# Kernel tuning notes

Measured on AMD Instinct MI355X. Metric: run time of the kernel, lower is better.

The kernel has to match this reference:

```python
import jax, jax.numpy as jnp
import numpy as np

B, N, D, H = 2, 2048, 256, 4
DH = D // H  # 64
ALPHA_DIV = 0.01
LN_EPS = 1e-5


def _split_heads(t):
    # [B, N, D] -> [B, H, N, DH]
    b, n, _ = t.shape
    return t.reshape(b, n, H, DH).transpose(0, 2, 1, 3)


def _merge_heads(t):
    # [B, H, N, DH] -> [B, N, D]
    b, h, n, d = t.shape
    return t.transpose(0, 2, 1, 3).reshape(b, n, h * d)


def setup_inputs() -> dict:
    key = jax.random.key(0)
    ks = jax.random.split(key, 20)
    p = lambda k, shape: (jax.random.normal(k, shape, dtype=jnp.float32) * 0.02)
    return {
        "x0": jax.random.normal(ks[0], (B, N, D), dtype=jnp.float32),
        "x1": jax.random.normal(ks[1], (B, N, D), dtype=jnp.float32),
        "cross_mask0": jax.random.uniform(ks[2], (B, 1, N), dtype=jnp.float32),
        "cross_mask1": jax.random.uniform(ks[3], (B, 1, N), dtype=jnp.float32),
        # weights stored as [in, out]
        "Wqk": p(ks[4], (D, D)), "bqk": jnp.zeros((D,), jnp.float32),
        "Wv": p(ks[5], (D, D)), "bv": jnp.zeros((D,), jnp.float32),
        "Wo": p(ks[6], (D, D)), "bo": jnp.zeros((D,), jnp.float32),
        "W1": p(ks[7], (2 * D, 2 * D)), "b1": jnp.zeros((2 * D,), jnp.float32),
        "ln_g": jnp.ones((2 * D,), jnp.float32), "ln_b": jnp.zeros((2 * D,), jnp.float32),
        "W2": p(ks[8], (2 * D, D)), "b2": jnp.zeros((D,), jnp.float32),
    }


def _ffn(x, W1, b1, ln_g, ln_b, W2, b2):
    h = x @ W1 + b1
    mu = jnp.mean(h, -1, keepdims=True)
    var = jnp.var(h, -1, keepdims=True)
    h = (h - mu) * jax.lax.rsqrt(var + LN_EPS) * ln_g + ln_b
    h = jax.nn.gelu(h, approximate=False)
    return h @ W2 + b2


def cross_block(x0, x1, cross_mask0, cross_mask1, Wqk, bqk, Wv, bv, Wo, bo,
                W1, b1, ln_g, ln_b, W2, b2):
    s = (DH ** -0.5) ** 0.5  # scale applied to each of qk0, qk1
    qk0 = _split_heads(x0 @ Wqk + bqk) * s
    qk1 = _split_heads(x1 @ Wqk + bqk) * s
    v0 = _split_heads(x0 @ Wv + bv)
    v1 = _split_heads(x1 @ Wv + bv)

    sim = jnp.einsum('bhid,bhjd->bhij', qk0, qk1)  # [B,H,N0,N1]

    # cross masks: [B,1,N] -> broadcast [B,1,1,N] over heads and query rows
    bad0 = (cross_mask0[:, :, None, :] < ALPHA_DIV)  # masks keys of dir 1->0
    bad1 = (cross_mask1[:, :, None, :] < ALPHA_DIV)  # masks keys of dir 0->1

    attn01 = jax.nn.softmax(jnp.where(bad1, -jnp.inf, sim), axis=-1)             # [B,H,N0,N1]
    attn10 = jax.nn.softmax(jnp.where(bad0, -jnp.inf, sim.swapaxes(-2, -1)), axis=-1)  # [B,H,N1,N0]

    m0 = jnp.einsum('bhij,bhjd->bhid', attn01, v1)
    m1 = jnp.einsum('bhij,bhjd->bhid', attn10, v0)

    m0 = _merge_heads(m0) @ Wo + bo
    m1 = _merge_heads(m1) @ Wo + bo

    out0 = x0 + _ffn(jnp.concatenate([x0, m0], -1), W1, b1, ln_g, ln_b, W2, b2)
    out1 = x1 + _ffn(jnp.concatenate([x1, m1], -1), W1, b1, ln_g, ln_b, W2, b2)
    return out0, out1, attn01, attn10


def reference(x0, x1, cross_mask0, cross_mask1, Wqk, bqk, Wv, bv, Wo, bo,
              W1, b1, ln_g, ln_b, W2, b2):
    return cross_block(x0, x1, cross_mask0, cross_mask1, Wqk, bqk, Wv, bv,
                       Wo, bo, W1, b1, ln_g, ln_b, W2, b2)
```

## Files before the change

kernel.cpp:

```cpp
#include <hip/hip_runtime.h>
#include <hip/hip_bf16.h>
#include <math.h>

#define B 2
#define N 2048
#define D 256
#define H 4
#define DH 64
#define D2 512
#define BH 8
#define BKP 40

static constexpr float ALPHA_DIV = 0.01f;
static constexpr float LN_EPS = 1e-5f;
static constexpr float SCL = 0.35355339059327373f;

typedef __attribute__((ext_vector_type(4))) float f32x4;
typedef __attribute__((ext_vector_type(8))) short s16x8;

__global__ __launch_bounds__(256) void proj_kernel(
    const float* __restrict__ x0, const float* __restrict__ x1,
    const __hip_bfloat16* __restrict__ WcT, const float* __restrict__ cb,
    __hip_bfloat16* __restrict__ qkv0, __hip_bfloat16* __restrict__ qkv1,
    __hip_bfloat16* __restrict__ vT,
    __hip_bfloat16* __restrict__ xc0, __hip_bfloat16* __restrict__ xc1)
{
    __shared__ __hip_bfloat16 As[128][BKP];
    __shared__ __hip_bfloat16 Ws[64][BKP];
    __shared__ __hip_bfloat16 T[128][72];
    const int z = blockIdx.z;
    const float* x = z ? x1 : x0;
    __hip_bfloat16* qkv = z ? qkv1 : qkv0;
    __hip_bfloat16* xc = z ? xc1 : xc0;
    const int rowBase = blockIdx.y * 128;
    const int colBase = blockIdx.x * 64;
    const int tid = threadIdx.x;
    const int lane = tid & 63, wid = tid >> 6;
    const int wr = wid >> 1, wc = wid & 1;
    const int lr = lane & 15, g = lane >> 4, lk = g * 8;

    f32x4 acc[4][2] = {};
    for (int k0 = 0; k0 < D; k0 += 32) {
#pragma unroll
        for (int c = 0; c < 2; c++) {
            int e = (tid + c * 256) * 8;
            int r = e >> 5, kk = e & 31;
            const float4 v0 = *(const float4*)&x[(size_t)(rowBase + r) * D + k0 + kk];
            const float4 v1 = *(const float4*)&x[(size_t)(rowBase + r) * D + k0 + kk + 4];
            union { s16x8 v; __hip_bfloat16 hh[8]; } u;
            u.hh[0] = __float2bfloat16(v0.x); u.hh[1] = __float2bfloat16(v0.y);
            u.hh[2] = __float2bfloat16(v0.z); u.hh[3] = __float2bfloat16(v0.w);
            u.hh[4] = __float2bfloat16(v1.x); u.hh[5] = __float2bfloat16(v1.y);
            u.hh[6] = __float2bfloat16(v1.z); u.hh[7] = __float2bfloat16(v1.w);
            *(s16x8*)&As[r][kk] = u.v;
            if (colBase == 0)
                *(s16x8*)&xc[(size_t)(rowBase + r) * D2 + k0 + kk] = u.v;
        }
        {
            int e = tid * 8;
            int n = e >> 5, kk = e & 31;
            *(s16x8*)&Ws[n][kk] = *(const s16x8*)&WcT[(size_t)(colBase + n) * D + k0 + kk];
        }
        __syncthreads();
        s16x8 a[4], b[2];
#pragma unroll
        for (int i = 0; i < 4; i++) a[i] = *(const s16x8*)&As[wr * 64 + i * 16 + lr][lk];
#pragma unroll
        for (int j = 0; j < 2; j++) b[j] = *(const s16x8*)&Ws[wc * 32 + j * 16 + lr][lk];
#pragma unroll
        for (int i = 0; i < 4; i++)
#pragma unroll
            for (int j = 0; j < 2; j++)
                acc[i][j] = __builtin_amdgcn_mfma_f32_16x16x32_bf16(a[i], b[j], acc[i][j], 0, 0, 0);
        __syncthreads();
    }

    if (colBase < 256) {
#pragma unroll
        for (int i = 0; i < 4; i++)
#pragma unroll
            for (int j = 0; j < 2; j++) {
                int col = colBase + wc * 32 + j * 16 + lr;
                float bval = cb[col];
#pragma unroll
                for (int t = 0; t < 4; t++) {
                    int row = rowBase + wr * 64 + i * 16 + g * 4 + t;
                    qkv[(size_t)row * D2 + col] = __float2bfloat16(acc[i][j][t] + bval);
                }
            }
    } else {
#pragma unroll
        for (int i = 0; i < 4; i++)
#pragma unroll
            for (int j = 0; j < 2; j++) {
                int cl = wc * 32 + j * 16 + lr;
                float bval = cb[colBase + cl];
#pragma unroll
                for (int t = 0; t < 4; t++)
                    T[wr * 64 + i * 16 + g * 4 + t][cl] = __float2bfloat16(acc[i][j][t] + bval);
            }
        __syncthreads();
        int hh = (colBase - 256) >> 6;
        int b_ = rowBase >> 11, n0 = rowBase & (N - 1);
        int slot = (z ? 0 : 8) + b_ * H + hh;
        int dh = tid >> 2, nn0 = (tid & 3) * 32;
        alignas(16) __hip_bfloat16 tmp[32];
#pragma unroll
        for (int u = 0; u < 32; u++) tmp[u] = T[nn0 + u][dh];
        __hip_bfloat16* dst = vT + ((size_t)slot * DH + dh) * N + n0 + nn0;
#pragma unroll
        for (int u8 = 0; u8 < 4; u8++)
            *(s16x8*)&dst[u8 * 8] = *(s16x8*)&tmp[u8 * 8];
    }
}

__device__ void transpose_tile(const float* W, int ldw, __hip_bfloat16* WT, int ldt,
                               int n0, int k0, float scale)
{
    __shared__ float T[32][33];
    int t = threadIdx.x;
    int r = t >> 3, c = (t & 7) * 4;
    float4 v = *(const float4*)&W[(size_t)(k0 + r) * ldw + n0 + c];
    T[r][c] = v.x; T[r][c + 1] = v.y; T[r][c + 2] = v.z; T[r][c + 3] = v.w;
    __syncthreads();
    __hip_bfloat16* dst = &WT[(size_t)(n0 + r) * ldt + k0 + c];
    dst[0] = __float2bfloat16(T[c][r] * scale);
    dst[1] = __float2bfloat16(T[c + 1][r] * scale);
    dst[2] = __float2bfloat16(T[c + 2][r] * scale);
    dst[3] = __float2bfloat16(T[c + 3][r] * scale);
}

__global__ __launch_bounds__(256) void prep_weights(
    const float* Wqk, const float* Wv, const float* Wo,
    const float* W1, const float* W2,
    const float* bqk, const float* bv, const float* b1, const float* bo,
    __hip_bfloat16* WcT, __hip_bfloat16* W1cT, __hip_bfloat16* W2T,
    float* cb, float* cb2)
{
    int blk = blockIdx.x;
    if (blk < 64) {
        int nT = blk & 7, kT = blk >> 3;
        transpose_tile(Wqk, 256, WcT, 256, nT * 32, kT * 32, SCL);
    } else if (blk < 128) {
        int t = blk - 64; int nT = t & 7, kT = t >> 3;
        transpose_tile(Wv, 256, WcT + 256 * 256, 256, nT * 32, kT * 32, 1.f);
    } else if (blk < 256) {
        int t = blk - 128; int nT = t & 15, kT = t >> 4;
        transpose_tile(W1, 512, W1cT, 512, nT * 32, kT * 32, 1.f);
    } else if (blk < 384) {
        int t = blk - 256; int nT = t & 7, kT = t >> 3;
        transpose_tile(W2, 256, W2T, 512, nT * 32, kT * 32, 1.f);
    } else if (blk < 416) {
        __shared__ float As[64][17];
        __shared__ float Bs[64][17];
        int t2 = blk - 384;
        int n0 = (t2 & 7) * 64, k0 = (t2 >> 3) * 64;
        int tx = threadIdx.x & 15, ty = threadIdx.x >> 4;
        float acc[4][4] = {};
        for (int c0 = 0; c0 < 256; c0 += 16) {
#pragma unroll
            for (int it = 0; it < 4; it++) {
                int idx = threadIdx.x + it * 256;
                int n = idx & 63, c = idx >> 6;
                As[n][c] = W1[(size_t)(256 + c0 + c) * 512 + n0 + n];
            }
#pragma unroll
            for (int it = 0; it < 4; it++) {
                int idx = threadIdx.x + it * 256;
                int k = idx >> 4, c = idx & 15;
                Bs[k][c] = Wo[(size_t)(k0 + k) * 256 + c0 + c];
            }
            __syncthreads();
#pragma unroll
            for (int c = 0; c < 16; c++) {
                float av[4], bv2[4];
#pragma unroll
                for (int i = 0; i < 4; i++) av[i] = As[ty + i * 16][c];
#pragma unroll
                for (int j = 0; j < 4; j++) bv2[j] = Bs[tx + j * 16][c];
#pragma unroll
                for (int i = 0; i < 4; i++)
#pragma unroll
                    for (int j = 0; j < 4; j++) acc[i][j] += av[i] * bv2[j];
            }
            __syncthreads();
        }
#pragma unroll
        for (int i = 0; i < 4; i++)
#pragma unroll
            for (int j = 0; j < 4; j++)
                W1cT[(size_t)(n0 + ty + i * 16) * 512 + 256 + k0 + tx + j * 16] =
                    __float2bfloat16(acc[i][j]);
    } else if (blk < 418) {
        int n = (blk - 416) * 256 + threadIdx.x;
        float s = b1[n];
        for (int c = 0; c < 256; c++) s += bo[c] * W1[(size_t)(256 + c) * 512 + n];
        cb2[n] = s;
    } else {
        int t = threadIdx.x;
        cb[t] = SCL * bqk[t];
        cb[256 + t] = bv[t];
    }
}

__global__ __launch_bounds__(256) void fused_attn_av(
    const __hip_bfloat16* __restrict__ qkv0, const __hip_bfloat16* __restrict__ qkv1,
    const float* __restrict__ cm0, const float* __restrict__ cm1,
    const __hip_bfloat16* __restrict__ vT,
    float* __restrict__ attn01, float* __restrict__ attn10,
    __hip_bfloat16* __restrict__ xc0, __hip_bfloat16* __restrict__ xc1)
{
    __shared__ __hip_bfloat16 Kt[128][72];
    __shared__ __hip_bfloat16 Pfb[64][136];
    __shared__ float okm[2048];

    const int tid = threadIdx.x;
    int l = blockIdx.x;
    int xcd = l & 7, idx = l >> 3;
    int zz = xcd * 2 + (idx >> 5);
    int xb = idx & 31;
    int dir = zz >> 3, bh = zz & 7;
    int b = bh >> 2, h = bh & 3;

    const __hip_bfloat16* qQ = (dir ? qkv1 : qkv0) + (size_t)b * N * D2 + h * DH;
    const __hip_bfloat16* qK = (dir ? qkv0 : qkv1) + (size_t)b * N * D2 + h * DH;
    const float* cmK = (dir ? cm0 : cm1) + b * N;
    const __hip_bfloat16* vslot = vT + (size_t)((dir ? 8 : 0) + bh) * DH * N;
    float* attnOut = (dir ? attn10 : attn01) + (size_t)bh * N * N;
    __hip_bfloat16* mOut = (dir ? xc1 : xc0) + (size_t)b * N * D2 + 256 + h * DH;

    const int i0 = xb * 64;
    const int lane = tid & 63, w = tid >> 6;
    const int lr = lane & 15, g = lane >> 4;

    s16x8 a0 = *(const s16x8*)&qQ[(size_t)(i0 + w * 16 + lr) * D2 + g * 8];
    s16x8 a1 = *(const s16x8*)&qQ[(size_t)(i0 + w * 16 + lr) * D2 + 32 + g * 8];

#pragma unroll
    for (int it = 0; it < 8; it++) okm[tid + it * 256] = cmK[tid + it * 256];

    s16x8 kreg[4];
    auto loadK = [&](int jt) {
        const int kk0 = jt * 128;
#pragma unroll
        for (int c = 0; c < 4; c++) {
            int e = (tid + c * 256) * 8;
            kreg[c] = *(const s16x8*)&qK[(size_t)(kk0 + (e >> 6)) * D2 + (e & 63)];
        }
    };
    auto writeK = [&]() {
#pragma unroll
        for (int c = 0; c < 4; c++) {
            int e = (tid + c * 256) * 8;
            *(s16x8*)&Kt[e >> 6][e & 63] = kreg[c];
        }
    };

    float sp[4] = { 0.f, 0.f, 0.f, 0.f };
    loadK(0);
    for (int jt = 0; jt < 16; jt++) {
        writeK();
        __syncthreads();
        if (jt < 15) loadK(jt + 1);

        f32x4 accs[8] = {};
#pragma unroll
        for (int j = 0; j < 8; j++) {
            s16x8 bb = *(const s16x8*)&Kt[j * 16 + lr][g * 8];
            accs[j] = __builtin_amdgcn_mfma_f32_16x16x32_bf16(a0, bb, accs[j], 0, 0, 0);
        }
#pragma unroll
        for (int j = 0; j < 8; j++) {
            s16x8 bb = *(const s16x8*)&Kt[j * 16 + lr][32 + g * 8];
            accs[j] = __builtin_amdgcn_mfma_f32_16x16x32_bf16(a1, bb, accs[j], 0, 0, 0);
        }
        const int k0 = jt * 128;
#pragma unroll
        for (int j = 0; j < 8; j++) {
            bool ok = okm[k0 + j * 16 + lr] >= ALPHA_DIV;
#pragma unroll
            for (int t = 0; t < 4; t++)
                if (ok) sp[t] += __expf(accs[j][t]);
        }
        __syncthreads();
    }
    float inv[4];
#pragma unroll
    for (int t = 0; t < 4; t++) {
#pragma unroll
        for (int off = 1; off <= 8; off <<= 1) sp[t] += __shfl_xor(sp[t], off);
        inv[t] = 1.f / sp[t];
    }

    f32x4 acc_o[4] = {};
    loadK(0);
    for (int jt = 0; jt < 16; jt++) {
        writeK();
        __syncthreads();
        if (jt < 15) loadK(jt + 1);
        const int k0 = jt * 128;

        s16x8 vf[4][4];
#pragma unroll
        for (int ks = 0; ks < 4; ks++)
#pragma unroll
            for (int j = 0; j < 4; j++)
                vf[ks][j] = *(const s16x8*)&vslot[(size_t)(j * 16 + lr) * N + k0 + ks * 32 + g * 8];

        f32x4 accs[8] = {};
#pragma unroll
        for (int j = 0; j < 8; j++) {
            s16x8 bb = *(const s16x8*)&Kt[j * 16 + lr][g * 8];
            accs[j] = __builtin_amdgcn_mfma_f32_16x16x32_bf16(a0, bb, accs[j], 0, 0, 0);
        }
#pragma unroll
        for (int j = 0; j < 8; j++) {
            s16x8 bb = *(const s16x8*)&Kt[j * 16 + lr][32 + g * 8];
            accs[j] = __builtin_amdgcn_mfma_f32_16x16x32_bf16(a1, bb, accs[j], 0, 0, 0);
        }

#pragma unroll
        for (int j = 0; j < 8; j++) {
            bool ok = okm[k0 + j * 16 + lr] >= ALPHA_DIV;
#pragma unroll
            for (int t = 0; t < 4; t++) {
                float pv = ok ? __expf(accs[j][t]) * inv[t] : 0.f;
                Pfb[w * 16 + g * 4 + t][j * 16 + lr] = __float2bfloat16(pv);
            }
        }
        __syncthreads();

#pragma unroll
        for (int k = 0; k < 4; k++) {
            int f = tid + k * 256;
            int r = f >> 4, c0 = (f & 15) * 8;
            union { s16x8 v; __hip_bfloat16 hh[8]; } u;
            u.v = *(const s16x8*)&Pfb[r][c0];
            float4 o0, o1;
            o0.x = __bfloat162float(u.hh[0]); o0.y = __bfloat162float(u.hh[1]);
            o0.z = __bfloat162float(u.hh[2]); o0.w = __bfloat162float(u.hh[3]);
            o1.x = __bfloat162float(u.hh[4]); o1.y = __bfloat162float(u.hh[5]);
            o1.z = __bfloat162float(u.hh[6]); o1.w = __bfloat162float(u.hh[7]);
            *(float4*)&attnOut[(size_t)(i0 + r) * N + k0 + c0] = o0;
            *(float4*)&attnOut[(size_t)(i0 + r) * N + k0 + c0 + 4] = o1;
        }

#pragma unroll
        for (int ks = 0; ks < 4; ks++) {
            s16x8 pa = *(const s16x8*)&Pfb[w * 16 + lr][ks * 32 + g * 8];
#pragma unroll
            for (int j = 0; j < 4; j++)
                acc_o[j] = __builtin_amdgcn_mfma_f32_16x16x32_bf16(pa, vf[ks][j], acc_o[j], 0, 0, 0);
        }
        __syncthreads();
    }

    __hip_bfloat16* Ob = (__hip_bfloat16*)Pfb;
#pragma unroll
    for (int j = 0; j < 4; j++)
#pragma unroll
        for (int t = 0; t < 4; t++)
            Ob[(w * 16 + g * 4 + t) * 136 + j * 16 + lr] = __float2bfloat16(acc_o[j][t]);
    __syncthreads();
    {
        int row = tid >> 2, c0 = (tid & 3) * 16;
        *(s16x8*)&mOut[(size_t)(i0 + row) * D2 + c0]     = *(const s16x8*)&Ob[row * 136 + c0];
        *(s16x8*)&mOut[(size_t)(i0 + row) * D2 + c0 + 8] = *(const s16x8*)&Ob[row * 136 + c0 + 8];
    }
}

#define HS_LD 528
__global__ __launch_bounds__(256) void ffn_tail(
    const __hip_bfloat16* __restrict__ xc0, const __hip_bfloat16* __restrict__ xc1,
    const __hip_bfloat16* __restrict__ W1T, const float* __restrict__ b1,
    const float* __restrict__ lng, const float* __restrict__ lnb,
    const __hip_bfloat16* __restrict__ W2T, const float* __restrict__ b2,
    const float* __restrict__ x0, const float* __restrict__ x1,
    float* __restrict__ out0, float* __restrict__ out1)
{
    __shared__ __hip_bfloat16 As[32][BKP];
    __shared__ __hip_bfloat16 WH[512 * BKP];
    __shared__ float redS[4][32], redQ[4][32];

    const __hip_bfloat16* xc = blockIdx.y ? xc1 : xc0;
    const float* xres = blockIdx.y ? x1 : x0;
    float* outp = blockIdx.y ? out1 : out0;
    const int rowBase = blockIdx.x * 32;
    const int tid = threadIdx.x;
    const int w = tid >> 6, lane = tid & 63;
    const int lr = lane & 15, g = lane >> 4, lk = g * 8;

    f32x4 acc[2][8] = {};
    for (int k0 = 0; k0 < D2; k0 += 32) {
        if (tid < 128) {
            int e = tid * 8;
            int r = e >> 5, kk = e & 31;
            *(s16x8*)&As[r][kk] = *(const s16x8*)&xc[(size_t)(rowBase + r) * D2 + k0 + kk];
        }
#pragma unroll
        for (int c = 0; c < 8; c++) {
            int e = (tid + c * 256) * 8;
            int n = e >> 5, kk = e & 31;
            *(s16x8*)&WH[n * BKP + kk] = *(const s16x8*)&W1T[(size_t)n * D2 + k0 + kk];
        }
        __syncthreads();
        s16x8 a[2], b[8];
#pragma unroll
        for (int i = 0; i < 2; i++) a[i] = *(const s16x8*)&As[i * 16 + lr][lk];
#pragma unroll
        for (int j = 0; j < 8; j++) b[j] = *(const s16x8*)&WH[(w * 128 + j * 16 + lr) * BKP + lk];
#pragma unroll
        for (int i = 0; i < 2; i++)
#pragma unroll
            for (int j = 0; j < 8; j++)
                acc[i][j] = __builtin_amdgcn_mfma_f32_16x16x32_bf16(a[i], b[j], acc[i][j], 0, 0, 0);
        __syncthreads();
    }

    float cols_b[8];
#pragma unroll
    for (int j = 0; j < 8; j++) cols_b[j] = b1[w * 128 + j * 16 + lr];
#pragma unroll
    for (int i = 0; i < 2; i++) {
#pragma unroll
        for (int t = 0; t < 4; t++) {
            float s = 0.f, q = 0.f;
#pragma unroll
            for (int j = 0; j < 8; j++) {
                float hv = acc[i][j][t] + cols_b[j];
                acc[i][j][t] = hv;
                s += hv; q += hv * hv;
            }
#pragma unroll
            for (int off = 1; off <= 8; off <<= 1) {
                s += __shfl_xor(s, off);
                q += __shfl_xor(q, off);
            }
            if (lr == 0) {
                int row = i * 16 + g * 4 + t;
                redS[w][row] = s; redQ[w][row] = q;
            }
        }
    }
    __syncthreads();

    __hip_bfloat16* Hs = WH;
    float gcol[8], bcol[8];
#pragma unroll
    for (int j = 0; j < 8; j++) {
        gcol[j] = lng[w * 128 + j * 16 + lr];
        bcol[j] = lnb[w * 128 + j * 16 + lr];
    }
#pragma unroll
    for (int i = 0; i < 2; i++) {
#pragma unroll
        for (int t = 0; t < 4; t++) {
            int row = i * 16 + g * 4 + t;
            float sum = redS[0][row] + redS[1][row] + redS[2][row] + redS[3][row];
            float sq  = redQ[0][row] + redQ[1][row] + redQ[2][row] + redQ[3][row];
            float mu = sum * (1.f / 512.f);
            float var = sq * (1.f / 512.f) - mu * mu;
            float rstd = rsqrtf(var + LN_EPS);
#pragma unroll
            for (int j = 0; j < 8; j++) {
                float y = (acc[i][j][t] - mu) * rstd * gcol[j] + bcol[j];
                float ge = 0.5f * y * (1.f + erff(y * 0.70710678118654752f));
                Hs[row * HS_LD + w * 128 + j * 16 + lr] = __float2bfloat16(ge);
            }
        }
    }
    __syncthreads();

    f32x4 acc2[2][4] = {};
    for (int k0 = 0; k0 < D2; k0 += 32) {
        s16x8 a[2], b[4];
#pragma unroll
        for (int i = 0; i < 2; i++)
            a[i] = *(const s16x8*)&Hs[(i * 16 + lr) * HS_LD + k0 + lk];
#pragma unroll
        for (int j = 0; j < 4; j++)
            b[j] = *(const s16x8*)&W2T[(size_t)(w * 64 + j * 16 + lr) * D2 + k0 + lk];
#pragma unroll
        for (int i = 0; i < 2; i++)
#pragma unroll
            for (int j = 0; j < 4; j++)
                acc2[i][j] = __builtin_amdgcn_mfma_f32_16x16x32_bf16(a[i], b[j], acc2[i][j], 0, 0, 0);
    }
#pragma unroll
    for (int i = 0; i < 2; i++) {
#pragma unroll
        for (int j = 0; j < 4; j++) {
            int col = w * 64 + j * 16 + lr;
            float bval = b2[col];
#pragma unroll
            for (int t = 0; t < 4; t++) {
                int row = rowBase + i * 16 + g * 4 + t;
                outp[(size_t)row * D + col] =
                    acc2[i][j][t] + bval + xres[(size_t)row * D + col];
            }
        }
    }
}

extern "C" void kernel_launch(void* const* d_in, const int* in_sizes, int n_in,
                              void* d_out, int out_size, void* d_ws, size_t ws_size,
                              hipStream_t stream) {
    const float* x0  = (const float*)d_in[0];
    const float* x1  = (const float*)d_in[1];
    const float* cm0 = (const float*)d_in[2];
    const float* cm1 = (const float*)d_in[3];
    const float* Wqk = (const float*)d_in[4]; const float* bqk = (const float*)d_in[5];
    const float* Wv  = (const float*)d_in[6]; const float* bv  = (const float*)d_in[7];
    const float* Wo  = (const float*)d_in[8]; const float* bo  = (const float*)d_in[9];
    const float* W1  = (const float*)d_in[10]; const float* b1 = (const float*)d_in[11];
    const float* lng = (const float*)d_in[12]; const float* lnb = (const float*)d_in[13];
    const float* W2  = (const float*)d_in[14]; const float* b2 = (const float*)d_in[15];

    float* out = (float*)d_out;
    char* p = (char*)d_ws;

    const size_t XSZ = (size_t)B * N * D;
    auto alloc = [&](size_t bytes) { char* r = p; p += (bytes + 255) & ~255ull; return r; };
    __hip_bfloat16* qkv0 = (__hip_bfloat16*)alloc((size_t)B * N * D2 * 2);
    __hip_bfloat16* qkv1 = (__hip_bfloat16*)alloc((size_t)B * N * D2 * 2);
    __hip_bfloat16* vT   = (__hip_bfloat16*)alloc((size_t)16 * DH * N * 2);
    __hip_bfloat16* xc0  = (__hip_bfloat16*)alloc((size_t)B * N * D2 * 2);
    __hip_bfloat16* xc1  = (__hip_bfloat16*)alloc((size_t)B * N * D2 * 2);
    __hip_bfloat16* WcT  = (__hip_bfloat16*)alloc(512 * 256 * 2);
    __hip_bfloat16* W1cT = (__hip_bfloat16*)alloc(512 * 512 * 2);
    __hip_bfloat16* W2T  = (__hip_bfloat16*)alloc(256 * 512 * 2);
    float* cb            = (float*)alloc(512 * 4);
    float* cb2           = (float*)alloc(512 * 4);

    float* out0 = out;
    float* out1 = out + XSZ;
    float* attn01 = out + 2 * XSZ;
    float* attn10 = attn01 + (size_t)BH * N * N;

    dim3 blk(256);

    prep_weights<<<419, blk, 0, stream>>>(Wqk, Wv, Wo, W1, W2, bqk, bv, b1, bo,
                                          WcT, W1cT, W2T, cb, cb2);

    proj_kernel<<<dim3(8, 32, 2), blk, 0, stream>>>(
        x0, x1, WcT, cb, qkv0, qkv1, vT, xc0, xc1);

    fused_attn_av<<<512, blk, 0, stream>>>(qkv0, qkv1, cm0, cm1, vT,
        attn01, attn10, xc0, xc1);

    ffn_tail<<<dim3(128, 2), blk, 0, stream>>>(
        xc0, xc1, W1cT, cb2, lng, lnb, W2T, b2, x0, x1, out0, out1);
}
```

Baseline: 189.0 us.

## Read K directly from global and make each wave own its P rows, dropping block barriers

Removes the shared-memory K tile and its double-buffered staging, so each wave loads its K fragments straight from global memory (relying on L1/L2 reuse across the four waves). The attention-probability write-out is remapped so every wave stores only its own 16 rows of the P buffer. That removes all per-iteration __syncthreads in both passes. V fragments are now loaded inside the MFMA loop instead of being prefetched ahead of the compute. The trade-off is redundant global/L1 traffic for K across waves and less latency hiding for the K and V loads.

```diff
diff --git a/kernel.cpp b/kernel.cpp
--- a/kernel.cpp
+++ b/kernel.cpp
@@ -210,7 +210,6 @@
     float* __restrict__ attn01, float* __restrict__ attn10,
     __hip_bfloat16* __restrict__ xc0, __hip_bfloat16* __restrict__ xc1)
 {
-    __shared__ __hip_bfloat16 Kt[128][72];
     __shared__ __hip_bfloat16 Pfb[64][136];
     __shared__ float okm[2048];
 
@@ -238,43 +237,20 @@
 
 #pragma unroll
     for (int it = 0; it < 8; it++) okm[tid + it * 256] = cmK[tid + it * 256];
-
-    s16x8 kreg[4];
-    auto loadK = [&](int jt) {
-        const int kk0 = jt * 128;
-#pragma unroll
-        for (int c = 0; c < 4; c++) {
-            int e = (tid + c * 256) * 8;
-            kreg[c] = *(const s16x8*)&qK[(size_t)(kk0 + (e >> 6)) * D2 + (e & 63)];
-        }
-    };
-    auto writeK = [&]() {
-#pragma unroll
-        for (int c = 0; c < 4; c++) {
-            int e = (tid + c * 256) * 8;
-            *(s16x8*)&Kt[e >> 6][e & 63] = kreg[c];
-        }
-    };
+    __syncthreads();
 
     float sp[4] = { 0.f, 0.f, 0.f, 0.f };
-    loadK(0);
     for (int jt = 0; jt < 16; jt++) {
-        writeK();
-        __syncthreads();
-        if (jt < 15) loadK(jt + 1);
-
+        const int k0 = jt * 128;
         f32x4 accs[8] = {};
 #pragma unroll
         for (int j = 0; j < 8; j++) {
-            s16x8 bb = *(const s16x8*)&Kt[j * 16 + lr][g * 8];
-            accs[j] = __builtin_amdgcn_mfma_f32_16x16x32_bf16(a0, bb, accs[j], 0, 0, 0);
-        }
-#pragma unroll
-        for (int j = 0; j < 8; j++) {
-            s16x8 bb = *(const s16x8*)&Kt[j * 16 + lr][32 + g * 8];
-            accs[j] = __builtin_amdgcn_mfma_f32_16x16x32_bf16(a1, bb, accs[j], 0, 0, 0);
-        }
-        const int k0 = jt * 128;
+            const __hip_bfloat16* kr = &qK[(size_t)(k0 + j * 16 + lr) * D2];
+            s16x8 bb0 = *(const s16x8*)&kr[g * 8];
+            s16x8 bb1 = *(const s16x8*)&kr[32 + g * 8];
+            accs[j] = __builtin_amdgcn_mfma_f32_16x16x32_bf16(a0, bb0, accs[j], 0, 0, 0);
+            accs[j] = __builtin_amdgcn_mfma_f32_16x16x32_bf16(a1, bb1, accs[j], 0, 0, 0);
+        }
 #pragma unroll
         for (int j = 0; j < 8; j++) {
             bool ok = okm[k0 + j * 16 + lr] >= ALPHA_DIV;
@@ -282,7 +258,6 @@
             for (int t = 0; t < 4; t++)
                 if (ok) sp[t] += __expf(accs[j][t]);
         }
-        __syncthreads();
     }
     float inv[4];
 #pragma unroll
@@ -293,30 +268,17 @@
     }
 
     f32x4 acc_o[4] = {};
-    loadK(0);
     for (int jt = 0; jt < 16; jt++) {
-        writeK();
-        __syncthreads();
-        if (jt < 15) loadK(jt + 1);
         const int k0 = jt * 128;
 
-        s16x8 vf[4][4];
-#pragma unroll
-        for (int ks = 0; ks < 4; ks++)
-#pragma unroll
-            for (int j = 0; j < 4; j++)
-                vf[ks][j] = *(const s16x8*)&vslot[(size_t)(j * 16 + lr) * N + k0 + ks * 32 + g * 8];
-
         f32x4 accs[8] = {};
 #pragma unroll
         for (int j = 0; j < 8; j++) {
-            s16x8 bb = *(const s16x8*)&Kt[j * 16 + lr][g * 8];
-            accs[j] = __builtin_amdgcn_mfma_f32_16x16x32_bf16(a0, bb, accs[j], 0, 0, 0);
-        }
-#pragma unroll
-        for (int j = 0; j < 8; j++) {
-            s16x8 bb = *(const s16x8*)&Kt[j * 16 + lr][32 + g * 8];
-            accs[j] = __builtin_amdgcn_mfma_f32_16x16x32_bf16(a1, bb, accs[j], 0, 0, 0);
+            const __hip_bfloat16* kr = &qK[(size_t)(k0 + j * 16 + lr) * D2];
+            s16x8 bb0 = *(const s16x8*)&kr[g * 8];
+            s16x8 bb1 = *(const s16x8*)&kr[32 + g * 8];
+            accs[j] = __builtin_amdgcn_mfma_f32_16x16x32_bf16(a0, bb0, accs[j], 0, 0, 0);
+            accs[j] = __builtin_amdgcn_mfma_f32_16x16x32_bf16(a1, bb1, accs[j], 0, 0, 0);
         }
 
 #pragma unroll
@@ -328,33 +290,35 @@
                 Pfb[w * 16 + g * 4 + t][j * 16 + lr] = __float2bfloat16(pv);
             }
         }
-        __syncthreads();
-
-#pragma unroll
-        for (int k = 0; k < 4; k++) {
-            int f = tid + k * 256;
-            int r = f >> 4, c0 = (f & 15) * 8;
-            union { s16x8 v; __hip_bfloat16 hh[8]; } u;
-            u.v = *(const s16x8*)&Pfb[r][c0];
-            float4 o0, o1;
-            o0.x = __bfloat162float(u.hh[0]); o0.y = __bfloat162float(u.hh[1]);
-            o0.z = __bfloat162float(u.hh[2]); o0.w = __bfloat162float(u.hh[3]);
-            o1.x = __bfloat162float(u.hh[4]); o1.y = __bfloat162float(u.hh[5]);
-            o1.z = __bfloat162float(u.hh[6]); o1.w = __bfloat162float(u.hh[7]);
-            *(float4*)&attnOut[(size_t)(i0 + r) * N + k0 + c0] = o0;
-            *(float4*)&attnOut[(size_t)(i0 + r) * N + k0 + c0 + 4] = o1;
+
+        {
+            int r = w * 16 + (lane >> 2), cs = (lane & 3) * 32;
+#pragma unroll
+            for (int u = 0; u < 4; u++) {
+                union { s16x8 v; __hip_bfloat16 hh[8]; } uu;
+                uu.v = *(const s16x8*)&Pfb[r][cs + u * 8];
+                float4 o0, o1;
+                o0.x = __bfloat162float(uu.hh[0]); o0.y = __bfloat162float(uu.hh[1]);
+                o0.z = __bfloat162float(uu.hh[2]); o0.w = __bfloat162float(uu.hh[3]);
+                o1.x = __bfloat162float(uu.hh[4]); o1.y = __bfloat162float(uu.hh[5]);
+                o1.z = __bfloat162float(uu.hh[6]); o1.w = __bfloat162float(uu.hh[7]);
+                *(float4*)&attnOut[(size_t)(i0 + r) * N + k0 + cs + u * 8] = o0;
+                *(float4*)&attnOut[(size_t)(i0 + r) * N + k0 + cs + u * 8 + 4] = o1;
+            }
         }
 
 #pragma unroll
         for (int ks = 0; ks < 4; ks++) {
             s16x8 pa = *(const s16x8*)&Pfb[w * 16 + lr][ks * 32 + g * 8];
 #pragma unroll
-            for (int j = 0; j < 4; j++)
-                acc_o[j] = __builtin_amdgcn_mfma_f32_16x16x32_bf16(pa, vf[ks][j], acc_o[j], 0, 0, 0);
-        }
-        __syncthreads();
-    }
-
+            for (int j = 0; j < 4; j++) {
+                s16x8 vb = *(const s16x8*)&vslot[(size_t)(j * 16 + lr) * N + k0 + ks * 32 + g * 8];
+                acc_o[j] = __builtin_amdgcn_mfma_f32_16x16x32_bf16(pa, vb, acc_o[j], 0, 0, 0);
+            }
+        }
+    }
+
+    __syncthreads();
     __hip_bfloat16* Ob = (__hip_bfloat16*)Pfb;
 #pragma unroll
     for (int j = 0; j < 4; j++)
```

After: 310.9 us. +64.5%, slower.
